# Kernel tuning notes

Hardware: AMD Instinct MI355X
Metric: run time of the kernel (lower is better)

Reference implementation:

```python
import jax, jax.numpy as jnp
import numpy as np

N_NODES = 50000
EPS = 1e-12  # F.normalize default eps


def setup_inputs() -> dict:
    key = jax.random.key(0)
    k1, k2, k3 = jax.random.split(key, 3)
    d_in, d_out, n_edges = 256, 256, 800000
    input_matrix = jax.random.normal(k1, (N_NODES, d_in), dtype=jnp.float32)
    adjacency_coo_matrix = jax.random.randint(k2, (2, n_edges), 0, N_NODES, dtype=jnp.int64)
    W = jax.random.normal(k3, (2 * d_in, d_out), dtype=jnp.float32) * (1.0 / np.sqrt(2 * d_in))
    b = jnp.zeros((d_out,), dtype=jnp.float32)
    return {"input_matrix": input_matrix, "adjacency_coo_matrix": adjacency_coo_matrix, "W": W, "b": b}


def reference(input_matrix, adjacency_coo_matrix, W, b):
    src = adjacency_coo_matrix[0]  # neighbor (source) node per edge
    dst = adjacency_coo_matrix[1]  # destination node per edge
    # mean aggregation of neighbor features onto each destination node
    neigh_sum = jax.ops.segment_sum(input_matrix[src], dst, num_segments=N_NODES)  # [N, d_in]
    deg = jax.ops.segment_sum(jnp.ones_like(dst, dtype=input_matrix.dtype), dst, num_segments=N_NODES)
    neigh_mean = neigh_sum / jnp.maximum(deg, 1.0)[:, None]
    # GraphSAGE: project concat(self, neighbor mean)
    h = jnp.concatenate([input_matrix, neigh_mean], axis=-1)  # [N, 2*d_in]
    out = jax.nn.relu(h @ W + b)  # [N, d_out]
    # F.normalize: row-wise L2 with eps clamp
    norm = jnp.maximum(jnp.linalg.norm(out, axis=-1, keepdims=True), EPS)
    return out / norm
```

## Files before the change

kernel.cpp:

```cpp
#include <hip/hip_runtime.h>
#include <hip/hip_fp16.h>
#include <math.h>

#define D 256
#define EPS 1e-12f

typedef __attribute__((ext_vector_type(8))) short bf16x8;
typedef __attribute__((ext_vector_type(4))) float f32x4;

__device__ __forceinline__ unsigned short f2bf(float f) {
    unsigned int u = __builtin_bit_cast(unsigned int, f);
    unsigned int r = u + 0x7fffu + ((u >> 16) & 1u);
    return (unsigned short)(r >> 16);
}
__device__ __forceinline__ float bf2f(unsigned short s) {
    unsigned int u = ((unsigned int)s) << 16;
    return __builtin_bit_cast(float, u);
}

__global__ void hist_kernel(const int* __restrict__ adj, int* __restrict__ deg, int E) {
    int i = blockIdx.x * blockDim.x + threadIdx.x;
    int stride = gridDim.x * blockDim.x;
    for (int e = i; e < E; e += stride) atomicAdd(&deg[adj[E + e]], 1);
}

__global__ __launch_bounds__(1024) void scan_local(const int* __restrict__ deg,
                                                   int* __restrict__ tmp,
                                                   int* __restrict__ bsum, int N) {
    __shared__ int buf[1024];
    int t = threadIdx.x;
    int i = blockIdx.x * 1024 + t;
    int v = (i < N) ? deg[i] : 0;
    buf[t] = v;
    __syncthreads();
#pragma unroll
    for (int off = 1; off < 1024; off <<= 1) {
        int add = (t >= off) ? buf[t - off] : 0;
        __syncthreads();
        buf[t] += add;
        __syncthreads();
    }
    if (i < N) tmp[i] = buf[t];
    if (t == 1023) bsum[blockIdx.x] = buf[t];
}

__global__ void scan_carry(int* __restrict__ bsum, int nb) {
    if (threadIdx.x == 0 && blockIdx.x == 0) {
        int run = 0;
        for (int b = 0; b < nb; b++) { int v = bsum[b]; bsum[b] = run; run += v; }
    }
}

__global__ void scan_apply(const int* __restrict__ deg, int* __restrict__ offs,
                           const int* __restrict__ bsum, int* __restrict__ cursor,
                           int N, int E) {
    int i = blockIdx.x * blockDim.x + threadIdx.x;
    if (i < N) {
        int excl = offs[i] - deg[i] + bsum[i >> 10];
        offs[i] = excl;
        cursor[i] = excl;
    }
    if (i == 0) offs[N] = E;
}

__global__ void fill_kernel(const int* __restrict__ adj, int* __restrict__ cursor,
                            int* __restrict__ csr, int E) {
    int i = blockIdx.x * blockDim.x + threadIdx.x;
    int stride = gridDim.x * blockDim.x;
    for (int e = i; e < E; e += stride) {
        int src = adj[e];
        int dst = adj[E + e];
        int pos = atomicAdd(&cursor[dst], 1);
        csr[pos] = src;
    }
}

__global__ void xhalf_kernel(const float* __restrict__ x, __half* __restrict__ xh, int total8) {
    int i = blockIdx.x * blockDim.x + threadIdx.x;
    if (i >= total8) return;
    const float4* p = (const float4*)x + (size_t)i * 2;
    float4 v0 = p[0];
    float4 v1 = p[1];
    __half2 h[4];
    h[0] = __floats2half2_rn(v0.x, v0.y);
    h[1] = __floats2half2_rn(v0.z, v0.w);
    h[2] = __floats2half2_rn(v1.x, v1.y);
    h[3] = __floats2half2_rn(v1.z, v1.w);
    *(uint4*)(xh + (size_t)i * 8) = *(const uint4*)h;
}

__global__ __launch_bounds__(256) void gather_kernel(const __half* __restrict__ xh,
                                                     const int* __restrict__ offs,
                                                     const int* __restrict__ csr,
                                                     float* __restrict__ acc, int N) {
    int wv = blockIdx.x * (blockDim.x >> 6) + (threadIdx.x >> 6);
    wv = __builtin_amdgcn_readfirstlane(wv);
    if (wv >= N) return;
    int lane = threadIdx.x & 63;
    int beg = offs[wv];
    int end = offs[wv + 1];
    const __half* xp = xh + (size_t)lane * 4;
    float s0 = 0.f, s1 = 0.f, s2 = 0.f, s3 = 0.f;
    int j = beg;
    for (; j + 8 <= end; j += 8) {
        int n[8];
#pragma unroll
        for (int u = 0; u < 8; u++) n[u] = csr[j + u];
        uint2 r[8];
#pragma unroll
        for (int u = 0; u < 8; u++) r[u] = *(const uint2*)(xp + (size_t)n[u] * D);
#pragma unroll
        for (int u = 0; u < 8; u++) {
            float2 fa = __half22float2(__builtin_bit_cast(__half2, r[u].x));
            float2 fb = __half22float2(__builtin_bit_cast(__half2, r[u].y));
            s0 += fa.x; s1 += fa.y; s2 += fb.x; s3 += fb.y;
        }
    }
    for (; j < end; ++j) {
        uint2 r = *(const uint2*)(xp + (size_t)csr[j] * D);
        float2 fa = __half22float2(__builtin_bit_cast(__half2, r.x));
        float2 fb = __half22float2(__builtin_bit_cast(__half2, r.y));
        s0 += fa.x; s1 += fa.y; s2 += fb.x; s3 += fb.y;
    }
    float inv = 1.0f / fmaxf((float)(end - beg), 1.0f);
    float4 o = make_float4(s0 * inv, s1 * inv, s2 * inv, s3 * inv);
    *(float4*)(acc + (size_t)wv * D + lane * 4) = o;
}

__global__ void wsplit_kernel(const float* __restrict__ W,
                              short* __restrict__ Wfh, short* __restrict__ Wfl) {
    int tid = blockIdx.x * blockDim.x + threadIdx.x;
    int k = tid >> 8;
    int n = tid & 255;
    float v = W[(size_t)k * D + n];
    unsigned short h = f2bf(v);
    unsigned short lo = f2bf(v - bf2f(h));
    int lane = (n & 15) | (((k >> 3) & 3) << 4);
    int idx = ((((n >> 4) << 4) + (k >> 5)) * 64 + lane) * 8 + (k & 7);
    Wfh[idx] = (short)h;
    Wfl[idx] = (short)lo;
}

__global__ __launch_bounds__(256) void gemm_mfma(
        const float* __restrict__ x,
        const float* __restrict__ acc,
        const short* __restrict__ Wfh,
        const short* __restrict__ Wfl,
        const float* __restrict__ bias,
        float* __restrict__ out,
        int N) {
    __shared__ short Ah[64][40];
    __shared__ short Al[64][40];
    __shared__ float ssbuf[4][64];

    int t = threadIdx.x;
    int w = t >> 6;
    int l = t & 63;
    int lg = l >> 4;
    int li = l & 15;
    int row0 = blockIdx.x * 64;

    f32x4 acc_[4][4];
#pragma unroll
    for (int mi = 0; mi < 4; mi++)
#pragma unroll
        for (int ni = 0; ni < 4; ni++)
            acc_[mi][ni] = (f32x4){0.f, 0.f, 0.f, 0.f};

    int srow = t >> 2;
    int skk = (t & 3) * 8;
    int gr = row0 + srow;
    int grc = gr < N ? gr : N - 1;

    for (int s = 0; s < 16; ++s) {
        int k0 = s * 32;
        bf16x8 bh[4], bl[4];
#pragma unroll
        for (int ni = 0; ni < 4; ni++) {
            int n16 = w * 4 + ni;
            size_t off = ((size_t)(n16 * 16 + s) * 64 + l) * 8;
            bh[ni] = *(const bf16x8*)(Wfh + off);
            bl[ni] = *(const bf16x8*)(Wfl + off);
        }

        __syncthreads();
        {
            const float* srcp = (k0 < D)
                ? (x + (size_t)grc * D + k0 + skk)
                : (acc + (size_t)grc * D + (k0 - D) + skk);
            float4 v0 = *(const float4*)(srcp);
            float4 v1 = *(const float4*)(srcp + 4);
            float vv[8] = {v0.x, v0.y, v0.z, v0.w, v1.x, v1.y, v1.z, v1.w};
            bf16x8 hv, lv;
#pragma unroll
            for (int j = 0; j < 8; j++) {
                unsigned short h = f2bf(vv[j]);
                hv[j] = (short)h;
                lv[j] = (short)f2bf(vv[j] - bf2f(h));
            }
            *(bf16x8*)&Ah[srow][skk] = hv;
            *(bf16x8*)&Al[srow][skk] = lv;
        }
        __syncthreads();

        bf16x8 ah[4], al[4];
#pragma unroll
        for (int mi = 0; mi < 4; mi++) {
            ah[mi] = *(const bf16x8*)&Ah[mi * 16 + li][lg * 8];
            al[mi] = *(const bf16x8*)&Al[mi * 16 + li][lg * 8];
        }

#pragma unroll
        for (int mi = 0; mi < 4; mi++)
#pragma unroll
            for (int ni = 0; ni < 4; ni++) {
                acc_[mi][ni] = __builtin_amdgcn_mfma_f32_16x16x32_bf16(ah[mi], bh[ni], acc_[mi][ni], 0, 0, 0);
                acc_[mi][ni] = __builtin_amdgcn_mfma_f32_16x16x32_bf16(ah[mi], bl[ni], acc_[mi][ni], 0, 0, 0);
                acc_[mi][ni] = __builtin_amdgcn_mfma_f32_16x16x32_bf16(al[mi], bh[ni], acc_[mi][ni], 0, 0, 0);
            }
    }

    float bv[4];
#pragma unroll
    for (int ni = 0; ni < 4; ni++) bv[ni] = bias[w * 64 + ni * 16 + li];

#pragma unroll
    for (int mi = 0; mi < 4; mi++) {
#pragma unroll
        for (int reg = 0; reg < 4; reg++) {
            float sp = 0.f;
#pragma unroll
            for (int ni = 0; ni < 4; ni++) {
                float v = acc_[mi][ni][reg] + bv[ni];
                v = fmaxf(v, 0.f);
                acc_[mi][ni][reg] = v;
                sp += v * v;
            }
            sp += __shfl_xor(sp, 1);
            sp += __shfl_xor(sp, 2);
            sp += __shfl_xor(sp, 4);
            sp += __shfl_xor(sp, 8);
            if (li == 0) ssbuf[w][mi * 16 + lg * 4 + reg] = sp;
        }
    }
    __syncthreads();
#pragma unroll
    for (int mi = 0; mi < 4; mi++) {
#pragma unroll
        for (int reg = 0; reg < 4; reg++) {
            int r = mi * 16 + lg * 4 + reg;
            float tot = ssbuf[0][r] + ssbuf[1][r] + ssbuf[2][r] + ssbuf[3][r];
            float inv = 1.0f / fmaxf(sqrtf(tot), EPS);
            int grr = row0 + r;
            if (grr < N) {
#pragma unroll
                for (int ni = 0; ni < 4; ni++)
                    out[(size_t)grr * D + w * 64 + ni * 16 + li] = acc_[mi][ni][reg] * inv;
            }
        }
    }
}

__global__ void zero_floats(float* __restrict__ a, size_t n4) {
    size_t i = (size_t)blockIdx.x * blockDim.x + threadIdx.x;
    size_t stride = (size_t)gridDim.x * blockDim.x;
    float4* a4 = (float4*)a;
    float4 z = make_float4(0.f, 0.f, 0.f, 0.f);
    for (size_t k = i; k < n4; k += stride) a4[k] = z;
}

__global__ void scatter_kernel(const float* __restrict__ x, const int* __restrict__ adj,
                               float* __restrict__ acc, float* __restrict__ deg, int E) {
    int wave = blockIdx.x * (blockDim.x >> 6) + (threadIdx.x >> 6);
    int lane = threadIdx.x & 63;
    int nw = gridDim.x * (blockDim.x >> 6);
    for (int e = wave; e < E; e += nw) {
        int src = adj[e];
        int dst = adj[E + e];
        float4 v = *(const float4*)(x + (size_t)src * D + lane * 4);
        float* p = acc + (size_t)dst * D + lane * 4;
        atomicAdd(p + 0, v.x);
        atomicAdd(p + 1, v.y);
        atomicAdd(p + 2, v.z);
        atomicAdd(p + 3, v.w);
        if (lane == 0) atomicAdd(deg + dst, 1.0f);
    }
}

__global__ void mean_kernel(float* __restrict__ acc, const float* __restrict__ deg, int N) {
    int wv = blockIdx.x * (blockDim.x >> 6) + (threadIdx.x >> 6);
    if (wv >= N) return;
    int lane = threadIdx.x & 63;
    float inv = 1.0f / fmaxf(deg[wv], 1.0f);
    float4* p = (float4*)(acc + (size_t)wv * D) + lane;
    float4 v = *p;
    v.x *= inv; v.y *= inv; v.z *= inv; v.w *= inv;
    *p = v;
}

__global__ __launch_bounds__(256) void gemm_fp32(
        const float* __restrict__ x, const float* __restrict__ acc,
        const float* __restrict__ W, const float* __restrict__ bias,
        float* __restrict__ out, int N) {
    __shared__ float Ast[32][64];
    __shared__ float Ws[32][D];
    int t = threadIdx.x;
    int row0 = blockIdx.x * 64;
    int tx = t & 15, ty = t >> 4;
    float accr[4][16];
#pragma unroll
    for (int i = 0; i < 4; i++)
#pragma unroll
        for (int j = 0; j < 16; j++) accr[i][j] = 0.f;
    int arow = t >> 3, akv = t & 7, wc = t & 63, wk0 = t >> 6;
    for (int k0 = 0; k0 < 2 * D; k0 += 32) {
        __syncthreads();
#pragma unroll
        for (int rr = 0; rr < 2; rr++) {
            int rl = arow + rr * 32;
            int gr = row0 + rl;
            int grc = gr < N ? gr : N - 1;
            float4 v = (k0 < D) ? *(const float4*)(x + (size_t)grc * D + k0 + akv * 4)
                                : *(const float4*)(acc + (size_t)grc * D + (k0 - D) + akv * 4);
            Ast[akv * 4 + 0][rl] = v.x; Ast[akv * 4 + 1][rl] = v.y;
            Ast[akv * 4 + 2][rl] = v.z; Ast[akv * 4 + 3][rl] = v.w;
        }
#pragma unroll
        for (int kk = 0; kk < 8; kk++) {
            int kr = wk0 + kk * 4;
            *(float4*)(&Ws[kr][wc * 4]) = *(const float4*)(W + (size_t)(k0 + kr) * D + wc * 4);
        }
        __syncthreads();
#pragma unroll
        for (int k = 0; k < 32; k++) {
            float4 a4 = *(const float4*)(&Ast[k][ty * 4]);
            float av[4] = {a4.x, a4.y, a4.z, a4.w};
#pragma unroll
            for (int j2 = 0; j2 < 4; j2++) {
                float4 w4 = *(const float4*)(&Ws[k][j2 * 64 + tx * 4]);
                float wv[4] = {w4.x, w4.y, w4.z, w4.w};
#pragma unroll
                for (int i = 0; i < 4; i++)
#pragma unroll
                    for (int j = 0; j < 4; j++)
                        accr[i][j2 * 4 + j] += av[i] * wv[j];
            }
        }
    }
    float bval[16];
#pragma unroll
    for (int j2 = 0; j2 < 4; j2++) {
        float4 b4 = *(const float4*)(bias + j2 * 64 + tx * 4);
        bval[j2 * 4 + 0] = b4.x; bval[j2 * 4 + 1] = b4.y;
        bval[j2 * 4 + 2] = b4.z; bval[j2 * 4 + 3] = b4.w;
    }
#pragma unroll
    for (int i = 0; i < 4; i++) {
        float ss = 0.f;
#pragma unroll
        for (int j = 0; j < 16; j++) {
            float v = accr[i][j] + bval[j];
            v = fmaxf(v, 0.f);
            accr[i][j] = v;
            ss += v * v;
        }
        ss += __shfl_xor(ss, 1); ss += __shfl_xor(ss, 2);
        ss += __shfl_xor(ss, 4); ss += __shfl_xor(ss, 8);
        float inv = 1.0f / fmaxf(sqrtf(ss), EPS);
        int gr = row0 + ty * 4 + i;
        if (gr < N) {
#pragma unroll
            for (int j2 = 0; j2 < 4; j2++) {
                float4 o;
                o.x = accr[i][j2 * 4 + 0] * inv; o.y = accr[i][j2 * 4 + 1] * inv;
                o.z = accr[i][j2 * 4 + 2] * inv; o.w = accr[i][j2 * 4 + 3] * inv;
                *(float4*)(out + (size_t)gr * D + j2 * 64 + tx * 4) = o;
            }
        }
    }
}

extern "C" void kernel_launch(void* const* d_in, const int* in_sizes, int n_in,
                              void* d_out, int out_size, void* d_ws, size_t ws_size,
                              hipStream_t stream) {
    const float* x = (const float*)d_in[0];
    const int* adj = (const int*)d_in[1];
    const float* W = (const float*)d_in[2];
    const float* b = (const float*)d_in[3];
    float* out = (float*)d_out;

    int N = in_sizes[0] / D;
    int E = in_sizes[1] / 2;

    size_t accBytes = (size_t)N * D * sizeof(float);
    size_t nInts = (size_t)3 * N + 1 + E + 64;
    size_t intBytes = nInts * sizeof(int);
    size_t wElems = (size_t)2 * D * D;
    size_t wfBytes = 2 * wElems * sizeof(short);
    size_t xhBytes = (size_t)N * D * sizeof(__half);

    int gb = (N + 63) / 64;
    int gatherBlocks = (N + 3) / 4;
    int nbScan = (N + 1023) / 1024;
    int wsplitBlocks = (int)(wElems / 256);
    int xh8 = N * D / 8;

    auto run_csr_mfma = [&](float* acc, char* base) {
        int* deg = (int*)base;
        int* offs = deg + N;
        int* cursor = offs + N + 1;
        int* csr = cursor + N;
        int* bsum = csr + E;
        uintptr_t p2 = ((uintptr_t)(bsum + 64) + 15) & ~(uintptr_t)15;
        short* Wfh = (short*)p2;
        short* Wfl = Wfh + wElems;
        __half* xh = (__half*)(Wfl + wElems);
        hipMemsetAsync(deg, 0, (size_t)N * sizeof(int), stream);
        hist_kernel<<<1024, 256, 0, stream>>>(adj, deg, E);
        xhalf_kernel<<<(xh8 + 255) / 256, 256, 0, stream>>>(x, xh, xh8);
        scan_local<<<nbScan, 1024, 0, stream>>>(deg, offs, bsum, N);
        scan_carry<<<1, 64, 0, stream>>>(bsum, nbScan);
        scan_apply<<<(N + 255) / 256, 256, 0, stream>>>(deg, offs, bsum, cursor, N, E);
        fill_kernel<<<1024, 256, 0, stream>>>(adj, cursor, csr, E);
        gather_kernel<<<gatherBlocks, 256, 0, stream>>>(xh, offs, csr, acc, N);
        wsplit_kernel<<<wsplitBlocks, 256, 0, stream>>>(W, Wfh, Wfl);
        gemm_mfma<<<gb, 256, 0, stream>>>(x, acc, Wfh, Wfl, b, out, N);
    };

    if (ws_size >= accBytes + intBytes + wfBytes + xhBytes + 32) {
        run_csr_mfma((float*)d_ws, (char*)d_ws + accBytes);
    } else if (ws_size >= intBytes + wfBytes + xhBytes + 32) {
        run_csr_mfma((float*)d_out, (char*)d_ws);
    } else {
        float* acc = (float*)d_out;
        float* deg = (float*)d_ws;
        zero_floats<<<2048, 256, 0, stream>>>(acc, (size_t)N * D / 4);
        zero_floats<<<64, 256, 0, stream>>>(deg, (size_t)N / 4);
        scatter_kernel<<<2048, 256, 0, stream>>>(x, adj, acc, deg, E);
        mean_kernel<<<gatherBlocks, 256, 0, stream>>>(acc, deg, N);
        gemm_fp32<<<gb, 256, 0, stream>>>(x, acc, W, b, out, N);
    }
}
```

Measured before the change: 337.4 us.

## Fuse neighbor gather into GEMM kernel and merge prep kernels

Moves the mean-aggregation gather into the GEMM kernel: each block gathers its 64 rows' neighbor means into shared memory as fp16, then feeds them into the bf16-split MFMA loop, removing the fp32 N×D intermediate write and re-read. Merges histogram, fp16 conversion of x and the W split into one grid-stride prep kernel. Replaces the serial scan_carry launch with a per-thread prefix loop in scan_apply. The trade-off is that the gather now runs inside the GEMM blocks, with only 782 blocks and about 34KB of LDS each, which can reduce occupancy and latency hiding for the random gathers. The neighbor mean also gets an extra fp16 rounding before the bf16 split.

```diff
diff --git a/kernel.cpp b/kernel.cpp
--- a/kernel.cpp
+++ b/kernel.cpp
@@ -4,6 +4,7 @@
 
 #define D 256
 #define EPS 1e-12f
+#define MP 264
 
 typedef __attribute__((ext_vector_type(8))) short bf16x8;
 typedef __attribute__((ext_vector_type(4))) float f32x4;
@@ -18,10 +19,42 @@
     return __builtin_bit_cast(float, u);
 }
 
-__global__ void hist_kernel(const int* __restrict__ adj, int* __restrict__ deg, int E) {
-    int i = blockIdx.x * blockDim.x + threadIdx.x;
+__global__ void prep_kernel(const int* __restrict__ adj, int* __restrict__ deg,
+                            const float* __restrict__ x, __half* __restrict__ xh,
+                            const float* __restrict__ W,
+                            short* __restrict__ Wfh, short* __restrict__ Wfl,
+                            int E, int total8) {
+    int tid = blockIdx.x * blockDim.x + threadIdx.x;
     int stride = gridDim.x * blockDim.x;
-    for (int e = i; e < E; e += stride) atomicAdd(&deg[adj[E + e]], 1);
+    int wsplitN = 2 * D * D;
+    int total = E + total8 + wsplitN;
+    for (int i = tid; i < total; i += stride) {
+        if (i < E) {
+            atomicAdd(&deg[adj[E + i]], 1);
+        } else if (i < E + total8) {
+            int q = i - E;
+            const float4* p = (const float4*)x + (size_t)q * 2;
+            float4 v0 = p[0];
+            float4 v1 = p[1];
+            __half2 h[4];
+            h[0] = __floats2half2_rn(v0.x, v0.y);
+            h[1] = __floats2half2_rn(v0.z, v0.w);
+            h[2] = __floats2half2_rn(v1.x, v1.y);
+            h[3] = __floats2half2_rn(v1.z, v1.w);
+            *(uint4*)(xh + (size_t)q * 8) = *(const uint4*)h;
+        } else {
+            int q = i - E - total8;
+            int k = q >> 8;
+            int n = q & 255;
+            float v = W[(size_t)k * D + n];
+            unsigned short h = f2bf(v);
+            unsigned short lo = f2bf(v - bf2f(h));
+            int lane = (n & 15) | (((k >> 3) & 3) << 4);
+            int idx = ((((n >> 4) << 4) + (k >> 5)) * 64 + lane) * 8 + (k & 7);
+            Wfh[idx] = (short)h;
+            Wfl[idx] = (short)lo;
+        }
+    }
 }
 
 __global__ __launch_bounds__(1024) void scan_local(const int* __restrict__ deg,
@@ -44,19 +77,15 @@
     if (t == 1023) bsum[blockIdx.x] = buf[t];
 }
 
-__global__ void scan_carry(int* __restrict__ bsum, int nb) {
-    if (threadIdx.x == 0 && blockIdx.x == 0) {
-        int run = 0;
-        for (int b = 0; b < nb; b++) { int v = bsum[b]; bsum[b] = run; run += v; }
-    }
-}
-
 __global__ void scan_apply(const int* __restrict__ deg, int* __restrict__ offs,
                            const int* __restrict__ bsum, int* __restrict__ cursor,
                            int N, int E) {
     int i = blockIdx.x * blockDim.x + threadIdx.x;
     if (i < N) {
-        int excl = offs[i] - deg[i] + bsum[i >> 10];
+        int chunk = i >> 10;
+        int carry = 0;
+        for (int b = 0; b < chunk; ++b) carry += bsum[b];
+        int excl = offs[i] - deg[i] + carry;
         offs[i] = excl;
         cursor[i] = excl;
     }
@@ -75,80 +104,17 @@
     }
 }
 
-__global__ void xhalf_kernel(const float* __restrict__ x, __half* __restrict__ xh, int total8) {
-    int i = blockIdx.x * blockDim.x + threadIdx.x;
-    if (i >= total8) return;
-    const float4* p = (const float4*)x + (size_t)i * 2;
-    float4 v0 = p[0];
-    float4 v1 = p[1];
-    __half2 h[4];
-    h[0] = __floats2half2_rn(v0.x, v0.y);
-    h[1] = __floats2half2_rn(v0.z, v0.w);
-    h[2] = __floats2half2_rn(v1.x, v1.y);
-    h[3] = __floats2half2_rn(v1.z, v1.w);
-    *(uint4*)(xh + (size_t)i * 8) = *(const uint4*)h;
-}
-
-__global__ __launch_bounds__(256) void gather_kernel(const __half* __restrict__ xh,
-                                                     const int* __restrict__ offs,
-                                                     const int* __restrict__ csr,
-                                                     float* __restrict__ acc, int N) {
-    int wv = blockIdx.x * (blockDim.x >> 6) + (threadIdx.x >> 6);
-    wv = __builtin_amdgcn_readfirstlane(wv);
-    if (wv >= N) return;
-    int lane = threadIdx.x & 63;
-    int beg = offs[wv];
-    int end = offs[wv + 1];
-    const __half* xp = xh + (size_t)lane * 4;
-    float s0 = 0.f, s1 = 0.f, s2 = 0.f, s3 = 0.f;
-    int j = beg;
-    for (; j + 8 <= end; j += 8) {
-        int n[8];
-#pragma unroll
-        for (int u = 0; u < 8; u++) n[u] = csr[j + u];
-        uint2 r[8];
-#pragma unroll
-        for (int u = 0; u < 8; u++) r[u] = *(const uint2*)(xp + (size_t)n[u] * D);
-#pragma unroll
-        for (int u = 0; u < 8; u++) {
-            float2 fa = __half22float2(__builtin_bit_cast(__half2, r[u].x));
-            float2 fb = __half22float2(__builtin_bit_cast(__half2, r[u].y));
-            s0 += fa.x; s1 += fa.y; s2 += fb.x; s3 += fb.y;
-        }
-    }
-    for (; j < end; ++j) {
-        uint2 r = *(const uint2*)(xp + (size_t)csr[j] * D);
-        float2 fa = __half22float2(__builtin_bit_cast(__half2, r.x));
-        float2 fb = __half22float2(__builtin_bit_cast(__half2, r.y));
-        s0 += fa.x; s1 += fa.y; s2 += fb.x; s3 += fb.y;
-    }
-    float inv = 1.0f / fmaxf((float)(end - beg), 1.0f);
-    float4 o = make_float4(s0 * inv, s1 * inv, s2 * inv, s3 * inv);
-    *(float4*)(acc + (size_t)wv * D + lane * 4) = o;
-}
-
-__global__ void wsplit_kernel(const float* __restrict__ W,
-                              short* __restrict__ Wfh, short* __restrict__ Wfl) {
-    int tid = blockIdx.x * blockDim.x + threadIdx.x;
-    int k = tid >> 8;
-    int n = tid & 255;
-    float v = W[(size_t)k * D + n];
-    unsigned short h = f2bf(v);
-    unsigned short lo = f2bf(v - bf2f(h));
-    int lane = (n & 15) | (((k >> 3) & 3) << 4);
-    int idx = ((((n >> 4) << 4) + (k >> 5)) * 64 + lane) * 8 + (k & 7);
-    Wfh[idx] = (short)h;
-    Wfl[idx] = (short)lo;
-}
-
-__global__ __launch_bounds__(256) void gemm_mfma(
+__global__ __launch_bounds__(256) void fused_kernel(
         const float* __restrict__ x,
-        const float* __restrict__ acc,
+        const __half* __restrict__ xh,
+        const int* __restrict__ offs,
+        const int* __restrict__ csr,
         const short* __restrict__ Wfh,
         const short* __restrict__ Wfl,
         const float* __restrict__ bias,
         float* __restrict__ out,
         int N) {
+    __shared__ __half meanh[64 * MP];
     __shared__ short Ah[64][40];
     __shared__ short Al[64][40];
     __shared__ float ssbuf[4][64];
@@ -160,6 +126,45 @@
     int li = l & 15;
     int row0 = blockIdx.x * 64;
 
+    const __half* xp = xh + (size_t)l * 4;
+    for (int rr = 0; rr < 16; ++rr) {
+        int lr = w * 16 + rr;
+        int r = row0 + lr;
+        float s0 = 0.f, s1 = 0.f, s2 = 0.f, s3 = 0.f;
+        if (r < N) {
+            int beg = offs[r];
+            int end = offs[r + 1];
+            int j = beg;
+            for (; j + 8 <= end; j += 8) {
+                int n[8];
+#pragma unroll
+                for (int u = 0; u < 8; u++) n[u] = csr[j + u];
+                uint2 rv[8];
+#pragma unroll
+                for (int u = 0; u < 8; u++) rv[u] = *(const uint2*)(xp + (size_t)n[u] * D);
+#pragma unroll
+                for (int u = 0; u < 8; u++) {
+                    float2 fa = __half22float2(__builtin_bit_cast(__half2, rv[u].x));
+                    float2 fb = __half22float2(__builtin_bit_cast(__half2, rv[u].y));
+                    s0 += fa.x; s1 += fa.y; s2 += fb.x; s3 += fb.y;
+                }
+            }
+            for (; j < end; ++j) {
+                uint2 rv = *(const uint2*)(xp + (size_t)csr[j] * D);
+                float2 fa = __half22float2(__builtin_bit_cast(__half2, rv.x));
+                float2 fb = __half22float2(__builtin_bit_cast(__half2, rv.y));
+                s0 += fa.x; s1 += fa.y; s2 += fb.x; s3 += fb.y;
+            }
+            float inv = 1.0f / fmaxf((float)(end - beg), 1.0f);
+            s0 *= inv; s1 *= inv; s2 *= inv; s3 *= inv;
+        }
+        uint2 pk;
+        pk.x = __builtin_bit_cast(unsigned int, __floats2half2_rn(s0, s1));
+        pk.y = __builtin_bit_cast(unsigned int, __floats2half2_rn(s2, s3));
+        *(uint2*)&meanh[lr * MP + 4 * l] = pk;
+    }
+    __syncthreads();
+
     f32x4 acc_[4][4];
 #pragma unroll
     for (int mi = 0; mi < 4; mi++)
@@ -185,12 +190,22 @@
 
         __syncthreads();
         {
-            const float* srcp = (k0 < D)
-                ? (x + (size_t)grc * D + k0 + skk)
-                : (acc + (size_t)grc * D + (k0 - D) + skk);
-            float4 v0 = *(const float4*)(srcp);
-            float4 v1 = *(const float4*)(srcp + 4);
-            float vv[8] = {v0.x, v0.y, v0.z, v0.w, v1.x, v1.y, v1.z, v1.w};
+            float vv[8];
+            if (k0 < D) {
+                const float* srcp = x + (size_t)grc * D + k0 + skk;
+                float4 v0 = *(const float4*)(srcp);
+                float4 v1 = *(const float4*)(srcp + 4);
+                vv[0] = v0.x; vv[1] = v0.y; vv[2] = v0.z; vv[3] = v0.w;
+                vv[4] = v1.x; vv[5] = v1.y; vv[6] = v1.z; vv[7] = v1.w;
+            } else {
+                uint4 mr = *(const uint4*)&meanh[srow * MP + (k0 - D) + skk];
+                float2 f0 = __half22float2(__builtin_bit_cast(__half2, mr.x));
+                float2 f1 = __half22float2(__builtin_bit_cast(__half2, mr.y));
+                float2 f2 = __half22float2(__builtin_bit_cast(__half2, mr.z));
+                float2 f3 = __half22float2(__builtin_bit_cast(__half2, mr.w));
+                vv[0] = f0.x; vv[1] = f0.y; vv[2] = f1.x; vv[3] = f1.y;
+                vv[4] = f2.x; vv[5] = f2.y; vv[6] = f3.x; vv[7] = f3.y;
+            }
             bf16x8 hv, lv;
 #pragma unroll
             for (int j = 0; j < 8; j++) {
@@ -392,7 +407,6 @@
     int N = in_sizes[0] / D;
     int E = in_sizes[1] / 2;
 
-    size_t accBytes = (size_t)N * D * sizeof(float);
     size_t nInts = (size_t)3 * N + 1 + E + 64;
     size_t intBytes = nInts * sizeof(int);
     size_t wElems = (size_t)2 * D * D;
@@ -400,13 +414,11 @@
     size_t xhBytes = (size_t)N * D * sizeof(__half);
 
     int gb = (N + 63) / 64;
-    int gatherBlocks = (N + 3) / 4;
     int nbScan = (N + 1023) / 1024;
-    int wsplitBlocks = (int)(wElems / 256);
-    int xh8 = N * D / 8;
-
-    auto run_csr_mfma = [&](float* acc, char* base) {
-        int* deg = (int*)base;
+    int total8 = N * D / 8;
+
+    if (ws_size >= intBytes + wfBytes + xhBytes + 32) {
+        int* deg = (int*)d_ws;
         int* offs = deg + N;
         int* cursor = offs + N + 1;
         int* csr = cursor + N;
@@ -415,25 +427,17 @@
         short* Wfh = (short*)p2;
         short* Wfl = Wfh + wElems;
         __half* xh = (__half*)(Wfl + wElems);
+
         hipMemsetAsync(deg, 0, (size_t)N * sizeof(int), stream);
-        hist_kernel<<<1024, 256, 0, stream>>>(adj, deg, E);
-        xhalf_kernel<<<(xh8 + 255) / 256, 256, 0, stream>>>(x, xh, xh8);
+        prep_kernel<<<2048, 256, 0, stream>>>(adj, deg, x, xh, W, Wfh, Wfl, E, total8);
         scan_local<<<nbScan, 1024, 0, stream>>>(deg, offs, bsum, N);
-        scan_carry<<<1, 64, 0, stream>>>(bsum, nbScan);
         scan_apply<<<(N + 255) / 256, 256, 0, stream>>>(deg, offs, bsum, cursor, N, E);
         fill_kernel<<<1024, 256, 0, stream>>>(adj, cursor, csr, E);
-        gather_kernel<<<gatherBlocks, 256, 0, stream>>>(xh, offs, csr, acc, N);
-        wsplit_kernel<<<wsplitBlocks, 256, 0, stream>>>(W, Wfh, Wfl);
-        gemm_mfma<<<gb, 256, 0, stream>>>(x, acc, Wfh, Wfl, b, out, N);
-    };
-
-    if (ws_size >= accBytes + intBytes + wfBytes + xhBytes + 32) {
-        run_csr_mfma((float*)d_ws, (char*)d_ws + accBytes);
-    } else if (ws_size >= intBytes + wfBytes + xhBytes + 32) {
-        run_csr_mfma((float*)d_out, (char*)d_ws);
+        fused_kernel<<<gb, 256, 0, stream>>>(x, xh, offs, csr, Wfh, Wfl, b, out, N);
     } else {
         float* acc = (float*)d_out;
         float* deg = (float*)d_ws;
+        int gatherBlocks = (N + 3) / 4;
         zero_floats<<<2048, 256, 0, stream>>>(acc, (size_t)N * D / 4);
         zero_floats<<<64, 256, 0, stream>>>(deg, (size_t)N / 4);
         scatter_kernel<<<2048, 256, 0, stream>>>(x, adj, acc, deg, E);
```

Measured after the change: 367.4 us. +8.9%, slower.
